# Optimization experiments

Measured on AMD Instinct MI355X. Metric: run time of the kernel, lower is better.

## Reference

```python
import jax, jax.numpy as jnp
import numpy as np

sigmoid = jax.nn.sigmoid

def lstm_layer(x_seq, W, U, b, act):
    """Keras-style LSTM. x_seq: [B,T,D], W: [D,4H], U: [H,4H], b: [4H].
    Gate order i,f,c,o. recurrent_activation=sigmoid, cell/output activation=act.
    Returns full hidden sequence [B,T,H]."""
    B, T, D = x_seq.shape
    H = U.shape[0]
    # precompute input contribution for all timesteps: [T,B,4H]
    xW = jnp.einsum('btd,dg->tbg', x_seq, W) + b
    h0 = jnp.zeros((B, H), x_seq.dtype)
    c0 = jnp.zeros((B, H), x_seq.dtype)

    def step(carry, xw_t):
        h, c = carry
        z = xw_t + h @ U  # [B,4H]
        i, f, g, o = jnp.split(z, 4, axis=-1)
        i = sigmoid(i)
        f = sigmoid(f)
        g = act(g)
        o = sigmoid(o)
        c_new = f * c + i * g
        h_new = o * act(c_new)
        return (h_new, c_new), h_new

    (_, _), hs = jax.lax.scan(step, (h0, c0), xW)  # hs: [T,B,H]
    return jnp.transpose(hs, (1, 0, 2))


def setup_inputs() -> dict:
    key = jax.random.key(0)
    ks = jax.random.split(key, 7)
    B, T, V, E, H1, H2 = 4096, 200, 30000, 32, 32, 1
    x = jax.random.randint(ks[0], (B, T), 0, V, dtype=jnp.int32)
    emb = jax.random.normal(ks[1], (V, E), jnp.float32) * 0.05
    W1 = jax.random.normal(ks[2], (E, 4 * H1), jnp.float32) * 0.1
    U1 = jax.random.normal(ks[3], (H1, 4 * H1), jnp.float32) * 0.1
    b1 = jnp.zeros((4 * H1,), jnp.float32)
    W2 = jax.random.normal(ks[4], (H1, 4 * H2), jnp.float32) * 0.1
    U2 = jax.random.normal(ks[5], (H2, 4 * H2), jnp.float32) * 0.1
    b2 = jnp.zeros((4 * H2,), jnp.float32)
    return {"x": x, "emb": emb, "W1": W1, "U1": U1, "b1": b1,
            "W2": W2, "U2": U2, "b2": b2}


def reference(x, emb, W1, U1, b1, W2, U2, b2):
    e = emb[x]                                   # [B,T,32] embedding lookup
    h1 = lstm_layer(e, W1, U1, b1, jnp.tanh)     # [B,T,32]
    h2 = lstm_layer(h1, W2, U2, b2, sigmoid)     # [B,T,1] (activation='sigmoid')
    return h2[:, -1, :]                          # return_sequences=False -> last step [B,1]
```

## Files before the change

### kernel.cpp

```cpp
#include <hip/hip_runtime.h>
#include <hip/hip_bf16.h>

#define DEV_INLINE __device__ __forceinline__

typedef float v2f __attribute__((ext_vector_type(2)));
typedef __fp16 h2v __attribute__((ext_vector_type(2)));

DEV_INLINE int rl_i(int v, int l) { return __builtin_amdgcn_readlane(v, l); }
DEV_INLINE float sigmoid_f(float x) { return __builtin_amdgcn_rcpf(1.0f + __expf(-x)); }

#if __has_builtin(__builtin_amdgcn_fdot2)
DEV_INLINE float fdot2(h2v a, h2v b, float c) { return __builtin_amdgcn_fdot2(a, b, c, false); }
#else
DEV_INLINE float fdot2(h2v a, h2v b, float c) {
    return fmaf((float)a[0], (float)b[0], fmaf((float)a[1], (float)b[1], c));
}
#endif

__global__ __launch_bounds__(128) void embw_kernel(
    const float* __restrict__ emb, const float* __restrict__ W1,
    const float* __restrict__ b1, float* __restrict__ embW)
{
    const int v = blockIdx.x, c = threadIdx.x;
    __shared__ float e[32];
    if (c < 32) e[c] = emb[v * 32 + c];
    __syncthreads();
    float acc = b1[c];
#pragma unroll
    for (int d = 0; d < 32; ++d) acc = fmaf(e[d], W1[d * 128 + c], acc);
    embW[v * 128 + ((c & 63) << 1) + (c >> 6)] = acc;
}

template<int MODE>
__global__ __launch_bounds__(256) void lstm_kernel(
    const int* __restrict__ x, const float* __restrict__ embW,
    const float* __restrict__ emb, const float* __restrict__ W1,
    const float* __restrict__ b1, const float* __restrict__ U1,
    const float* __restrict__ W2, const float* __restrict__ U2,
    const float* __restrict__ b2, float* __restrict__ out, int T)
{
    const int lane = threadIdx.x & 63;
    const int wave = threadIdx.x >> 6;
    const int b    = blockIdx.x * 4 + wave;
    const bool low = lane < 32;
    const int ca = lane, cb = lane + 64;

    h2v upa[16], upb[16];
#pragma unroll
    for (int m = 0; m < 16; ++m) {
        h2v ta, tb;
        ta[0] = (__fp16)U1[(2 * m) * 128 + ca];
        ta[1] = (__fp16)U1[(2 * m + 1) * 128 + ca];
        tb[0] = (__fp16)U1[(2 * m) * 128 + cb];
        tb[1] = (__fp16)U1[(2 * m + 1) * 128 + cb];
        upa[m] = ta; upb[m] = tb;
    }

    h2v wpa[16], wpb[16];
    float ba = 0.f, bb = 0.f;
    if constexpr (MODE == 1) {
#pragma unroll
        for (int m = 0; m < 16; ++m) {
            h2v ta, tb;
            ta[0] = (__fp16)W1[(2 * m) * 128 + ca];
            ta[1] = (__fp16)W1[(2 * m + 1) * 128 + ca];
            tb[0] = (__fp16)W1[(2 * m) * 128 + cb];
            tb[1] = (__fp16)W1[(2 * m + 1) * 128 + cb];
            wpa[m] = ta; wpb[m] = tb;
        }
        ba = b1[ca]; bb = b1[cb];
    }

    const int gsel = lane >> 4;
    const int e0 = lane & 15, e1 = (lane & 15) + 16;
    const float w2a = W2[e0 * 4 + gsel];
    const float w2b = W2[e1 * 4 + gsel];
    const float u2s = U2[gsel];
    const float b2s = b2[gsel];

    const int* xrow = x + b * T;

    float h = 0.f, c = 0.f, h2 = 0.f, c2 = 0.f;

    int idxA = __builtin_amdgcn_readfirstlane(xrow[0]);
    int idxB = __builtin_amdgcn_readfirstlane(xrow[1]);

    v2f zc;
    float ec[32];
    if constexpr (MODE == 0) {
        zc = reinterpret_cast<const v2f*>(embW)[idxA * 64 + lane];
    } else {
#pragma unroll
        for (int d = 0; d < 32; ++d) ec[d] = emb[idxA * 32 + d];
    }

#pragma unroll 2
    for (int t = 0; t < T; ++t) {
        v2f zn;
        float en[32];
        if constexpr (MODE == 0) {
            zn = reinterpret_cast<const v2f*>(embW)[idxB * 64 + lane];
        } else {
#pragma unroll
            for (int d = 0; d < 32; ++d) en[d] = emb[idxB * 32 + d];
        }
        idxB = __builtin_amdgcn_readfirstlane(xrow[(t + 2 < T) ? (t + 2) : (T - 1)]);

        float za0, zb0;
        if constexpr (MODE == 0) {
            za0 = zc.x; zb0 = zc.y;
        } else {
            za0 = ba; zb0 = bb;
#pragma unroll
            for (int m = 0; m < 16; ++m) {
                h2v ep = __builtin_amdgcn_cvt_pkrtz(ec[2 * m], ec[2 * m + 1]);
                za0 = fdot2(ep, wpa[m], za0);
                zb0 = fdot2(ep, wpb[m], zb0);
            }
        }
        float hx = __shfl_xor(h, 1);
        int hpi = __builtin_bit_cast(int, __builtin_amdgcn_cvt_pkrtz(h, hx));
        float za1 = 0.f, zb1 = 0.f;
#pragma unroll
        for (int m = 0; m < 16; m += 2) {
            h2v h0 = __builtin_bit_cast(h2v, rl_i(hpi, 2 * m));
            h2v h1 = __builtin_bit_cast(h2v, rl_i(hpi, 2 * m + 2));
            za0 = fdot2(h0, upa[m],     za0);
            zb0 = fdot2(h0, upb[m],     zb0);
            za1 = fdot2(h1, upa[m + 1], za1);
            zb1 = fdot2(h1, upb[m + 1], zb1);
        }
        const float za = za0 + za1;
        const float zb = zb0 + zb1;

        float sa = sigmoid_f(za);
        float xb_ = low ? 2.0f * zb : zb;
        float u  = sigmoid_f(xb_);
        float rb = low ? 2.0f * u - 1.0f : u;

        float sa_x = __shfl_xor(sa, 32);
        float rb_x = __shfl_xor(rb, 32);
        float iv = low ? sa   : sa_x;
        float fv = low ? sa_x : sa;
        float gv = low ? rb   : rb_x;
        float ov = low ? rb_x : rb;

        c = fmaf(fv, c, iv * gv);
        float tc = 2.0f * sigmoid_f(2.0f * c) - 1.0f;
        h = ov * tc;

        float ha = __shfl(h, e0);
        float hb = __shfl(h, e1);
        float p = ha * w2a + hb * w2b;
        p += __shfl_xor(p, 1);
        p += __shfl_xor(p, 2);
        p += __shfl_xor(p, 4);
        p += __shfl_xor(p, 8);
        float s2 = sigmoid_f(p + fmaf(u2s, h2, b2s));
        float i2 = __uint_as_float(rl_i(__float_as_uint(s2), 0));
        float f2 = __uint_as_float(rl_i(__float_as_uint(s2), 16));
        float g2 = __uint_as_float(rl_i(__float_as_uint(s2), 32));
        float o2 = __uint_as_float(rl_i(__float_as_uint(s2), 48));
        c2 = fmaf(f2, c2, i2 * g2);
        h2 = o2 * sigmoid_f(c2);

        if constexpr (MODE == 0) {
            zc = zn;
        } else {
#pragma unroll
            for (int d = 0; d < 32; ++d) ec[d] = en[d];
        }
    }

    if (lane == 0) out[b] = h2;
}

extern "C" void kernel_launch(void* const* d_in, const int* in_sizes, int n_in,
                              void* d_out, int out_size, void* d_ws, size_t ws_size,
                              hipStream_t stream) {
    const int*   x   = (const int*)d_in[0];
    const float* emb = (const float*)d_in[1];
    const float* W1  = (const float*)d_in[2];
    const float* U1  = (const float*)d_in[3];
    const float* b1  = (const float*)d_in[4];
    const float* W2  = (const float*)d_in[5];
    const float* U2  = (const float*)d_in[6];
    const float* b2  = (const float*)d_in[7];
    float* out = (float*)d_out;

    const int V = in_sizes[1] / 32;
    const int T = 200;
    const int B = in_sizes[0] / T;
    const int blocks = B / 4;

    const size_t need = (size_t)V * 128 * sizeof(float);
    if (ws_size >= need) {
        float* embW = (float*)d_ws;
        embw_kernel<<<V, 128, 0, stream>>>(emb, W1, b1, embW);
        lstm_kernel<0><<<blocks, 256, 0, stream>>>(x, embW, emb, W1, b1, U1,
                                                   W2, U2, b2, out, T);
    } else {
        lstm_kernel<1><<<blocks, 256, 0, stream>>>(x, nullptr, emb, W1, b1, U1,
                                                   W2, U2, b2, out, T);
    }
}
```

Before: 296.7 us.

## Reuse packed h broadcast for layer-2 dot, skew layer 2, use DPP/permlane

Layer 2 now consumes the scalar-broadcast fp16-packed h values already produced for the layer-1 recurrence, using fdot2 against packed W2 instead of shuffles plus a butterfly reduction. Layer 2's update is deferred by one step so it overlaps with the next step's layer-1 work, and a final update runs after the loop. Cross-lane exchanges switch to a DPP swap and permlane32_swap where available, replacing ds_bpermute-based shuffles. This adds fp16 rounding to the layer-2 input dot product and raises register pressure from the 16 packed h values and W2 weights.

Measured after the change: 293.3 us. No clear change (-1.1%).

```diff
diff --git a/kernel.cpp b/kernel.cpp
--- a/kernel.cpp
+++ b/kernel.cpp
@@ -7,6 +7,9 @@
 typedef __fp16 h2v __attribute__((ext_vector_type(2)));
 
 DEV_INLINE int rl_i(int v, int l) { return __builtin_amdgcn_readlane(v, l); }
+DEV_INLINE float rlf(float v, int l) {
+    return __uint_as_float(__builtin_amdgcn_readlane(__float_as_uint(v), l));
+}
 DEV_INLINE float sigmoid_f(float x) { return __builtin_amdgcn_rcpf(1.0f + __expf(-x)); }
 
 #if __has_builtin(__builtin_amdgcn_fdot2)
@@ -16,6 +19,25 @@
     return fmaf((float)a[0], (float)b[0], fmaf((float)a[1], (float)b[1], c));
 }
 #endif
+
+DEV_INLINE float dpp_swap1(float v) {
+    int r = __builtin_amdgcn_update_dpp(__float_as_int(v), __float_as_int(v),
+                                        0xB1, 0xF, 0xF, false);
+    return __int_as_float(r);
+}
+
+DEV_INLINE void bcast_halves(float v, bool low, float& lo_b, float& hi_b) {
+#if __has_builtin(__builtin_amdgcn_permlane32_swap)
+    auto r = __builtin_amdgcn_permlane32_swap(__float_as_uint(v), __float_as_uint(v),
+                                              false, false);
+    lo_b = __uint_as_float(r[0]);
+    hi_b = __uint_as_float(r[1]);
+#else
+    float vx = __shfl_xor(v, 32);
+    lo_b = low ? v : vx;
+    hi_b = low ? vx : v;
+#endif
+}
 
 __global__ __launch_bounds__(128) void embw_kernel(
     const float* __restrict__ emb, const float* __restrict__ W1,
@@ -72,15 +94,36 @@
     }
 
     const int gsel = lane >> 4;
-    const int e0 = lane & 15, e1 = (lane & 15) + 16;
-    const float w2a = W2[e0 * 4 + gsel];
-    const float w2b = W2[e1 * 4 + gsel];
+    h2v w2p[16];
+#pragma unroll
+    for (int m = 0; m < 16; ++m) {
+        h2v tw;
+        tw[0] = (__fp16)W2[(2 * m) * 4 + gsel];
+        tw[1] = (__fp16)W2[(2 * m + 1) * 4 + gsel];
+        w2p[m] = tw;
+    }
     const float u2s = U2[gsel];
     const float b2s = b2[gsel];
 
     const int* xrow = x + b * T;
 
     float h = 0.f, c = 0.f, h2 = 0.f, c2 = 0.f;
+    int hp[16];
+
+#define LAYER2_UPDATE()                                                        \
+    do {                                                                       \
+        float p0 = 0.f, p1 = 0.f;                                              \
+        _Pragma("unroll")                                                      \
+        for (int m = 0; m < 16; m += 2) {                                      \
+            p0 = fdot2(__builtin_bit_cast(h2v, hp[m]),     w2p[m],     p0);    \
+            p1 = fdot2(__builtin_bit_cast(h2v, hp[m + 1]), w2p[m + 1], p1);    \
+        }                                                                      \
+        float s2 = sigmoid_f((p0 + p1) + fmaf(u2s, h2, b2s));                  \
+        float i2 = rlf(s2, 0),  f2 = rlf(s2, 16);                              \
+        float g2 = rlf(s2, 32), o2 = rlf(s2, 48);                              \
+        c2 = fmaf(f2, c2, i2 * g2);                                            \
+        h2 = o2 * sigmoid_f(c2);                                               \
+    } while (0)
 
     int idxA = __builtin_amdgcn_readfirstlane(xrow[0]);
     int idxB = __builtin_amdgcn_readfirstlane(xrow[1]);
@@ -106,6 +149,11 @@
         }
         idxB = __builtin_amdgcn_readfirstlane(xrow[(t + 2 < T) ? (t + 2) : (T - 1)]);
 
+        float hx = dpp_swap1(h);
+        int hpi = __builtin_bit_cast(int, __builtin_amdgcn_cvt_pkrtz(h, hx));
+#pragma unroll
+        for (int m = 0; m < 16; ++m) hp[m] = rl_i(hpi, 2 * m);
+
         float za0, zb0;
         if constexpr (MODE == 0) {
             za0 = zc.x; zb0 = zc.y;
@@ -118,13 +166,11 @@
                 zb0 = fdot2(ep, wpb[m], zb0);
             }
         }
-        float hx = __shfl_xor(h, 1);
-        int hpi = __builtin_bit_cast(int, __builtin_amdgcn_cvt_pkrtz(h, hx));
         float za1 = 0.f, zb1 = 0.f;
 #pragma unroll
         for (int m = 0; m < 16; m += 2) {
-            h2v h0 = __builtin_bit_cast(h2v, rl_i(hpi, 2 * m));
-            h2v h1 = __builtin_bit_cast(h2v, rl_i(hpi, 2 * m + 2));
+            h2v h0 = __builtin_bit_cast(h2v, hp[m]);
+            h2v h1 = __builtin_bit_cast(h2v, hp[m + 1]);
             za0 = fdot2(h0, upa[m],     za0);
             zb0 = fdot2(h0, upb[m],     zb0);
             za1 = fdot2(h1, upa[m + 1], za1);
@@ -133,37 +179,21 @@
         const float za = za0 + za1;
         const float zb = zb0 + zb1;
 
+        if (t) LAYER2_UPDATE();
+
         float sa = sigmoid_f(za);
         float xb_ = low ? 2.0f * zb : zb;
         float u  = sigmoid_f(xb_);
         float rb = low ? 2.0f * u - 1.0f : u;
 
-        float sa_x = __shfl_xor(sa, 32);
-        float rb_x = __shfl_xor(rb, 32);
-        float iv = low ? sa   : sa_x;
-        float fv = low ? sa_x : sa;
-        float gv = low ? rb   : rb_x;
-        float ov = low ? rb_x : rb;
+        float iv, fv, gv, ov;
+        bcast_halves(sa, low, iv, fv);
+        bcast_halves(rb, low, gv, ov);
 
         c = fmaf(fv, c, iv * gv);
         float tc = 2.0f * sigmoid_f(2.0f * c) - 1.0f;
         h = ov * tc;
 
-        float ha = __shfl(h, e0);
-        float hb = __shfl(h, e1);
-        float p = ha * w2a + hb * w2b;
-        p += __shfl_xor(p, 1);
-        p += __shfl_xor(p, 2);
-        p += __shfl_xor(p, 4);
-        p += __shfl_xor(p, 8);
-        float s2 = sigmoid_f(p + fmaf(u2s, h2, b2s));
-        float i2 = __uint_as_float(rl_i(__float_as_uint(s2), 0));
-        float f2 = __uint_as_float(rl_i(__float_as_uint(s2), 16));
-        float g2 = __uint_as_float(rl_i(__float_as_uint(s2), 32));
-        float o2 = __uint_as_float(rl_i(__float_as_uint(s2), 48));
-        c2 = fmaf(f2, c2, i2 * g2);
-        h2 = o2 * sigmoid_f(c2);
-
         if constexpr (MODE == 0) {
             zc = zn;
         } else {
@@ -172,7 +202,16 @@
         }
     }
 
+    {
+        float hx = dpp_swap1(h);
+        int hpi = __builtin_bit_cast(int, __builtin_amdgcn_cvt_pkrtz(h, hx));
+#pragma unroll
+        for (int m = 0; m < 16; ++m) hp[m] = rl_i(hpi, 2 * m);
+        LAYER2_UPDATE();
+    }
+
     if (lane == 0) out[b] = h2;
+#undef LAYER2_UPDATE
 }
 
 extern "C" void kernel_launch(void* const* d_in, const int* in_sizes, int n_in,
```
